# Kernel tuning notes

Hardware: AMD Instinct MI355X
Metric: run time of the kernel (lower is better)

## Reference

```python
import jax, jax.numpy as jnp
import numpy as np

B, T, D, H = 4, 2048, 1024, 16
DK = D // H  # 64
EPS = 1e-5


def _rope(q, k, offset=0):
    # q, k: (B, H, T, DK). Standard rotate-half RoPE, base 10000.
    half = DK // 2
    inv_freq = 1.0 / (10000.0 ** (jnp.arange(0, half, dtype=jnp.float32) / half))
    pos = jnp.arange(q.shape[2], dtype=jnp.float32) + offset  # (T,)
    freqs = pos[:, None] * inv_freq[None, :]          # (T, half)
    cos = jnp.concatenate([jnp.cos(freqs)] * 2, -1)   # (T, DK)
    sin = jnp.concatenate([jnp.sin(freqs)] * 2, -1)

    def rot(x):
        x1, x2 = x[..., :half], x[..., half:]
        return jnp.concatenate([-x2, x1], axis=-1)

    q = q * cos + rot(q) * sin
    k = k * cos + rot(k) * sin
    return q, k


def setup_inputs() -> dict:
    key = jax.random.key(0)
    k0, k1, k2 = jax.random.split(key, 3)
    s = 0.02
    return {
        "x": jax.random.normal(k0, (B, T, D), jnp.float32),
        "ln_w": jnp.ones((D,), jnp.float32),
        "ln_b": jnp.zeros((D,), jnp.float32),
        "w_qkv": jax.random.normal(k1, (D, 3 * D), jnp.float32) * s,
        "b_qkv": jnp.zeros((3 * D,), jnp.float32),
        "w_o": jax.random.normal(k2, (D, D), jnp.float32) * s,
        "b_o": jnp.zeros((D,), jnp.float32),
    }


def reference(x, ln_w, ln_b, w_qkv, b_qkv, w_o, b_o):
    # LayerNorm
    mu = jnp.mean(x, axis=-1, keepdims=True)
    var = jnp.mean(jnp.square(x - mu), axis=-1, keepdims=True)
    h = (x - mu) * jax.lax.rsqrt(var + EPS) * ln_w + ln_b

    # Fused QKV projection -> (B, T, 3, H, DK) -> per-head (B, H, T, DK)
    qkv = (h @ w_qkv + b_qkv).reshape(B, T, 3, H, DK)
    q = qkv[:, :, 0].transpose(0, 2, 1, 3)
    k = qkv[:, :, 1].transpose(0, 2, 1, 3)
    v = qkv[:, :, 2].transpose(0, 2, 1, 3)

    q, k = _rope(q, k, offset=0)

    # Causal SDPA
    scale = 1.0 / np.sqrt(DK)
    scores = jnp.einsum("bhqd,bhkd->bhqk", q, k) * scale
    causal = jnp.tril(jnp.ones((T, T), dtype=bool))
    scores = jnp.where(causal, scores, jnp.finfo(scores.dtype).min)
    attn = jax.nn.softmax(scores, axis=-1)
    out = jnp.einsum("bhqk,bhkd->bhqd", attn, v)

    out = out.transpose(0, 2, 1, 3).reshape(B, T, D)
    return out @ w_o + b_o
```

## Files before the change

### kernel.cpp

```cpp
#include <hip/hip_runtime.h>
#include <math.h>

#define B_ 4
#define T_ 2048
#define D_ 1024
#define H_ 16
#define DK_ 64
#define EPS_ 1e-5f
#define LOG2E 1.44269504f

typedef __attribute__((ext_vector_type(4))) float f32x4;
typedef __attribute__((ext_vector_type(8))) short sv8;
typedef __attribute__((ext_vector_type(4))) short sv4;

__device__ __forceinline__ short f2bf(float f) {
  union { float f; unsigned u; } x; x.f = f;
  unsigned r = x.u + 0x7fffu + ((x.u >> 16) & 1u);
  return (short)(r >> 16);
}

__device__ __forceinline__ void gload16(const void* g, void* l) {
  __builtin_amdgcn_global_load_lds((const __attribute__((address_space(1))) void*)g,
                                   (__attribute__((address_space(3))) void*)l, 16, 0, 0);
}

__global__ __launch_bounds__(256) void rope_tab(float2* __restrict__ cs) {
  const int i = blockIdx.x * 256 + threadIdx.x;
  const int t = i >> 5, f = i & 31;
  const float inv = powf(10000.0f, -(float)f / 32.0f);
  float sn, cn;
  sincosf((float)t * inv, &sn, &cn);
  cs[i] = make_float2(cn, sn);
}

__global__ __launch_bounds__(256) void ln_kernel(const float* __restrict__ x,
                                                 const float* __restrict__ w,
                                                 const float* __restrict__ b,
                                                 short* __restrict__ h) {
  const int row = blockIdx.x;
  const float4 v = ((const float4*)(x + (size_t)row * D_))[threadIdx.x];
  float s  = v.x + v.y + v.z + v.w;
  float ss = v.x*v.x + v.y*v.y + v.z*v.z + v.w*v.w;
  #pragma unroll
  for (int o = 32; o > 0; o >>= 1) {
    s  += __shfl_down(s,  o);
    ss += __shfl_down(ss, o);
  }
  __shared__ float red[8];
  const int wid = threadIdx.x >> 6, lane = threadIdx.x & 63;
  if (lane == 0) { red[wid] = s; red[wid + 4] = ss; }
  __syncthreads();
  s  = red[0] + red[1] + red[2] + red[3];
  ss = red[4] + red[5] + red[6] + red[7];
  const float mu  = s * (1.0f / D_);
  const float var = ss * (1.0f / D_) - mu * mu;
  const float inv = rsqrtf(var + EPS_);
  const float4 wv = ((const float4*)w)[threadIdx.x];
  const float4 bv = ((const float4*)b)[threadIdx.x];
  sv4 o;
  o[0] = f2bf((v.x - mu) * inv * wv.x + bv.x);
  o[1] = f2bf((v.y - mu) * inv * wv.y + bv.y);
  o[2] = f2bf((v.z - mu) * inv * wv.z + bv.z);
  o[3] = f2bf((v.w - mu) * inv * wv.w + bv.w);
  ((sv4*)(h + (size_t)row * D_))[threadIdx.x] = o;
}

__global__ __launch_bounds__(256) void conv_t(const float* __restrict__ W,
                                              short* __restrict__ WT,
                                              int K, int N) {
  __shared__ float tile[32][33];
  const int k0 = blockIdx.y * 32, n0 = blockIdx.x * 32;
  const int tx = threadIdx.x & 31, ty = threadIdx.x >> 5;
  #pragma unroll
  for (int i = 0; i < 4; ++i) {
    const int k = ty * 4 + i;
    tile[k][tx] = W[(size_t)(k0 + k) * N + n0 + tx];
  }
  __syncthreads();
  #pragma unroll
  for (int i = 0; i < 4; ++i) {
    const int n = ty * 4 + i;
    WT[(size_t)(n0 + n) * K + k0 + tx] = f2bf(tile[tx][n]);
  }
}

#define GBM 128
#define GBN 128
#define GBK 32

__device__ __forceinline__ void gstage(const short* __restrict__ A,
                                       const short* __restrict__ BT,
                                       short* AsB, short* BsB,
                                       int tid, size_t aoff, size_t boff) {
  #pragma unroll
  for (int rr = 0; rr < 2; ++rr) {
    const int c = tid + rr * 256;
    const int row = c >> 2, co = (c & 3) * 8;
    gload16(A + aoff + (size_t)row * D_ + co, AsB + c * 8);
    gload16(BT + boff + (size_t)row * D_ + co, BsB + c * 8);
  }
}

__global__ __launch_bounds__(256) void gemm_qkv_rope(const short* __restrict__ A,
                                                     const short* __restrict__ BT,
                                                     const float* __restrict__ bias,
                                                     const float2* __restrict__ cs,
                                                     short* __restrict__ qb,
                                                     short* __restrict__ kb,
                                                     short* __restrict__ vt) {
  __shared__ __align__(16) short As[2][GBM][GBK];
  __shared__ __align__(16) short Bs[2][GBN][GBK];
  const int tid = threadIdx.x;
  const int l = tid & 63, g = l >> 4, lq = l & 15;
  const int wm = (tid >> 6) >> 1, wn = (tid >> 6) & 1;
  const int m0 = blockIdx.y * GBM, n0 = blockIdx.x * GBN;

  f32x4 acc[4][4] = {};

  gstage(A, BT, &As[0][0][0], &Bs[0][0][0], tid, (size_t)m0 * D_, (size_t)n0 * D_);
  int cur = 0;
  for (int k0 = 0; k0 < D_; k0 += GBK) {
    __syncthreads();
    if (k0 + GBK < D_)
      gstage(A, BT, &As[cur ^ 1][0][0], &Bs[cur ^ 1][0][0], tid,
             (size_t)m0 * D_ + k0 + GBK, (size_t)n0 * D_ + k0 + GBK);
    sv8 af[4], bf[4];
    #pragma unroll
    for (int mi = 0; mi < 4; ++mi) af[mi] = *(const sv8*)&As[cur][64 * wm + 16 * mi + lq][8 * g];
    #pragma unroll
    for (int ni = 0; ni < 4; ++ni) bf[ni] = *(const sv8*)&Bs[cur][64 * wn + 16 * ni + lq][8 * g];
    #pragma unroll
    for (int mi = 0; mi < 4; ++mi)
      #pragma unroll
      for (int ni = 0; ni < 4; ++ni)
        acc[mi][ni] = __builtin_amdgcn_mfma_f32_16x16x32_bf16(af[mi], bf[ni], acc[mi][ni], 0, 0, 0);
    cur ^= 1;
  }

  const int sec = n0 >> 10;
  if (sec < 2) {
    short* dst = (sec == 0) ? qb : kb;
    const float qs = (sec == 0) ? 0.125f * LOG2E : 1.0f;
    #pragma unroll
    for (int nA = 0; nA < 2; ++nA) {
      const int colA = n0 + 64 * wn + 16 * nA + lq;
      const float bA = bias[colA], bB = bias[colA + 32];
      const int clA = colA & 1023;
      const int f = 16 * nA + lq;
      #pragma unroll
      for (int mi = 0; mi < 4; ++mi) {
        const int rbase = m0 + 64 * wm + 16 * mi + 4 * g;
        #pragma unroll
        for (int r = 0; r < 4; ++r) {
          const int row = rbase + r, t = row & (T_ - 1);
          const float2 c_s = cs[t * 32 + f];
          const float x1 = acc[mi][nA][r] + bA;
          const float x2 = acc[mi][nA + 2][r] + bB;
          dst[(size_t)row * D_ + clA]      = f2bf((x1 * c_s.x - x2 * c_s.y) * qs);
          dst[(size_t)row * D_ + clA + 32] = f2bf((x2 * c_s.x + x1 * c_s.y) * qs);
        }
      }
    }
  } else {
    #pragma unroll
    for (int ni = 0; ni < 4; ++ni) {
      const int col = n0 + 64 * wn + 16 * ni + lq;
      const float bb = bias[col];
      const int cl = col & 1023;
      const int hh = cl >> 6, d = cl & 63;
      #pragma unroll
      for (int mi = 0; mi < 4; ++mi) {
        const int rbase = m0 + 64 * wm + 16 * mi + 4 * g;
        #pragma unroll
        for (int r = 0; r < 4; ++r) {
          const int row = rbase + r;
          const int bI = row >> 11, t = row & (T_ - 1);
          vt[((size_t)(bI * H_ + hh) * DK_ + d) * T_ + t] = f2bf(acc[mi][ni][r] + bb);
        }
      }
    }
  }
}

__global__ __launch_bounds__(256) void gemm_bf16(const short* __restrict__ A,
                                                 const short* __restrict__ BT,
                                                 const float* __restrict__ bias,
                                                 float* __restrict__ C,
                                                 int M, int N) {
  __shared__ __align__(16) short As[2][GBM][GBK];
  __shared__ __align__(16) short Bs[2][GBN][GBK];
  const int tid = threadIdx.x;
  const int l = tid & 63, g = l >> 4, lq = l & 15;
  const int wm = (tid >> 6) >> 1, wn = (tid >> 6) & 1;
  const int m0 = blockIdx.y * GBM, n0 = blockIdx.x * GBN;

  f32x4 acc[4][4] = {};

  gstage(A, BT, &As[0][0][0], &Bs[0][0][0], tid, (size_t)m0 * D_, (size_t)n0 * D_);
  int cur = 0;
  for (int k0 = 0; k0 < D_; k0 += GBK) {
    __syncthreads();
    if (k0 + GBK < D_)
      gstage(A, BT, &As[cur ^ 1][0][0], &Bs[cur ^ 1][0][0], tid,
             (size_t)m0 * D_ + k0 + GBK, (size_t)n0 * D_ + k0 + GBK);
    sv8 af[4], bf[4];
    #pragma unroll
    for (int mi = 0; mi < 4; ++mi) af[mi] = *(const sv8*)&As[cur][64 * wm + 16 * mi + lq][8 * g];
    #pragma unroll
    for (int ni = 0; ni < 4; ++ni) bf[ni] = *(const sv8*)&Bs[cur][64 * wn + 16 * ni + lq][8 * g];
    #pragma unroll
    for (int mi = 0; mi < 4; ++mi)
      #pragma unroll
      for (int ni = 0; ni < 4; ++ni)
        acc[mi][ni] = __builtin_amdgcn_mfma_f32_16x16x32_bf16(af[mi], bf[ni], acc[mi][ni], 0, 0, 0);
    cur ^= 1;
  }

  #pragma unroll
  for (int ni = 0; ni < 4; ++ni) {
    const int col = n0 + 64 * wn + 16 * ni + lq;
    const float bb = bias[col];
    #pragma unroll
    for (int mi = 0; mi < 4; ++mi) {
      const int rbase = m0 + 64 * wm + 16 * mi + 4 * g;
      #pragma unroll
      for (int r = 0; r < 4; ++r)
        C[(size_t)(rbase + r) * N + col] = acc[mi][ni][r] + bb;
    }
  }
}

__global__ __launch_bounds__(256) void flash_mfma(const short* __restrict__ qb,
                                                  const short* __restrict__ kb,
                                                  const short* __restrict__ vt,
                                                  short* __restrict__ out) {
  __shared__ __align__(16) short Ks[64][72];
  __shared__ __align__(16) short Vt[64][72];
  __shared__ __align__(16) short Ps[4][16][72];

  const int tid = threadIdx.x;
  const int w = tid >> 6, l = tid & 63, g = l >> 4, lq = l & 15;
  const int wg = blockIdx.x;
  const int pair = wg & 63, bx = wg >> 6;
  const int hh = pair & 15, b = pair >> 4;
  const int q0 = bx * 64;
  const int qrow = q0 + 16 * w + lq;

  const short* qp = qb + (size_t)(b * T_ + qrow) * D_ + hh * DK_;
  sv8 qf[2];
  qf[0] = *(const sv8*)(qp + 8 * g);
  qf[1] = *(const sv8*)(qp + 32 + 8 * g);

  f32x4 o[4] = {{0,0,0,0},{0,0,0,0},{0,0,0,0},{0,0,0,0}};
  float m_run = -INFINITY, l_run = 0.0f;

  const short* kbB = kb + (size_t)(b * T_) * D_ + hh * DK_;
  const short* vtB = vt + (size_t)(b * H_ + hh) * DK_ * T_;
  const int niter = bx + 1;

  const int skey = tid >> 3, sj = tid & 7;

  int4 kr0, kr1, vr0, vr1;
  {
    kr0 = *(const int4*)(kbB + (size_t)(skey)      * D_ + sj * 8);
    kr1 = *(const int4*)(kbB + (size_t)(skey + 32) * D_ + sj * 8);
    vr0 = *(const int4*)(vtB + (size_t)(skey)      * T_ + sj * 8);
    vr1 = *(const int4*)(vtB + (size_t)(skey + 32) * T_ + sj * 8);
  }

  for (int it = 0; it < niter; ++it) {
    const int kv0 = it * 64;
    __syncthreads();
    *(int4*)&Ks[skey][sj * 8]      = kr0;
    *(int4*)&Ks[skey + 32][sj * 8] = kr1;
    *(int4*)&Vt[skey][sj * 8]      = vr0;
    *(int4*)&Vt[skey + 32][sj * 8] = vr1;
    __syncthreads();

    if (it + 1 < niter) {
      const int nk = kv0 + 64;
      kr0 = *(const int4*)(kbB + (size_t)(nk + skey)      * D_ + sj * 8);
      kr1 = *(const int4*)(kbB + (size_t)(nk + skey + 32) * D_ + sj * 8);
      vr0 = *(const int4*)(vtB + (size_t)(skey)      * T_ + nk + sj * 8);
      vr1 = *(const int4*)(vtB + (size_t)(skey + 32) * T_ + nk + sj * 8);
    }

    float sv[4][4];
    #pragma unroll
    for (int kt = 0; kt < 4; ++kt) {
      f32x4 acc = {0, 0, 0, 0};
      #pragma unroll
      for (int s = 0; s < 2; ++s) {
        const sv8 kf = *(const sv8*)&Ks[kt * 16 + lq][32 * s + 8 * g];
        acc = __builtin_amdgcn_mfma_f32_16x16x32_bf16(kf, qf[s], acc, 0, 0, 0);
      }
      sv[kt][0] = acc[0]; sv[kt][1] = acc[1]; sv[kt][2] = acc[2]; sv[kt][3] = acc[3];
    }

    if (it == niter - 1) {
      #pragma unroll
      for (int kt = 0; kt < 4; ++kt)
        #pragma unroll
        for (int r = 0; r < 4; ++r) {
          const int key_abs = kv0 + kt * 16 + 4 * g + r;
          if (key_abs > qrow) sv[kt][r] = -INFINITY;
        }
    }

    float tm = -INFINITY;
    #pragma unroll
    for (int kt = 0; kt < 4; ++kt)
      #pragma unroll
      for (int r = 0; r < 4; ++r) tm = fmaxf(tm, sv[kt][r]);
    tm = fmaxf(tm, __shfl_xor(tm, 16));
    tm = fmaxf(tm, __shfl_xor(tm, 32));
    if (__any(tm > m_run + 8.0f)) {
      const float mn = fmaxf(m_run, tm);
      const float alpha = __builtin_amdgcn_exp2f(m_run - mn);
      l_run *= alpha;
      #pragma unroll
      for (int r = 0; r < 4; ++r) {
        const float ar = __shfl(alpha, 4 * g + r);
        o[0][r] *= ar; o[1][r] *= ar; o[2][r] *= ar; o[3][r] *= ar;
      }
      m_run = mn;
    }
    float psum = 0.0f;
    #pragma unroll
    for (int kt = 0; kt < 4; ++kt)
      #pragma unroll
      for (int r = 0; r < 4; ++r) {
        const float p = __builtin_amdgcn_exp2f(sv[kt][r] - m_run);
        sv[kt][r] = p;
        psum += p;
      }
    psum += __shfl_xor(psum, 16);
    psum += __shfl_xor(psum, 32);
    l_run += psum;

    #pragma unroll
    for (int kt = 0; kt < 4; ++kt) {
      unsigned pa_, pb_;
      asm("v_cvt_pk_bf16_f32 %0, %1, %2" : "=v"(pa_) : "v"(sv[kt][0]), "v"(sv[kt][1]));
      asm("v_cvt_pk_bf16_f32 %0, %1, %2" : "=v"(pb_) : "v"(sv[kt][2]), "v"(sv[kt][3]));
      int2 pk; pk.x = (int)pa_; pk.y = (int)pb_;
      *(int2*)&Ps[w][lq][kt * 16 + 4 * g] = pk;
    }

    #pragma unroll
    for (int s = 0; s < 2; ++s) {
      const sv8 pa = *(const sv8*)&Ps[w][lq][32 * s + 8 * g];
      #pragma unroll
      for (int dt = 0; dt < 4; ++dt) {
        const sv8 vb = *(const sv8*)&Vt[dt * 16 + lq][32 * s + 8 * g];
        o[dt] = __builtin_amdgcn_mfma_f32_16x16x32_bf16(pa, vb, o[dt], 0, 0, 0);
      }
    }
  }

  #pragma unroll
  for (int r = 0; r < 4; ++r) {
    const float li = __shfl(l_run, 4 * g + r);
    const float inv = 1.0f / li;
    const int qr = q0 + 16 * w + 4 * g + r;
    short* op = out + (size_t)(b * T_ + qr) * D_ + hh * DK_;
    #pragma unroll
    for (int dt = 0; dt < 4; ++dt)
      op[dt * 16 + lq] = f2bf(o[dt][r] * inv);
  }
}

extern "C" void kernel_launch(void* const* d_in, const int* in_sizes, int n_in,
                              void* d_out, int out_size, void* d_ws, size_t ws_size,
                              hipStream_t stream) {
  const float* x     = (const float*)d_in[0];
  const float* ln_w  = (const float*)d_in[1];
  const float* ln_b  = (const float*)d_in[2];
  const float* w_qkv = (const float*)d_in[3];
  const float* b_qkv = (const float*)d_in[4];
  const float* w_o   = (const float*)d_in[5];
  const float* b_o   = (const float*)d_in[6];
  float* outp = (float*)d_out;

  const int rows = B_ * T_;
  const size_t nHD = (size_t)rows * D_;

  short* h      = (short*)d_ws;
  short* qb     = h + nHD;
  short* kb     = qb + nHD;
  short* vt     = kb + nHD;
  short* att    = vt + nHD;
  short* wqkvT  = att + nHD;
  short* woT    = wqkvT + (size_t)D_ * 3 * D_;
  float2* csT   = (float2*)(woT + (size_t)D_ * D_);

  rope_tab<<<T_ * 32 / 256, 256, 0, stream>>>(csT);
  conv_t<<<dim3(3 * D_ / 32, D_ / 32), 256, 0, stream>>>(w_qkv, wqkvT, D_, 3 * D_);
  conv_t<<<dim3(D_ / 32, D_ / 32), 256, 0, stream>>>(w_o, woT, D_, D_);

  ln_kernel<<<rows, 256, 0, stream>>>(x, ln_w, ln_b, h);

  {
    dim3 grid(3 * D_ / GBN, rows / GBM);
    gemm_qkv_rope<<<grid, 256, 0, stream>>>(h, wqkvT, b_qkv, csT, qb, kb, vt);
  }

  {
    flash_mfma<<<(T_ / 64) * H_ * B_, 256, 0, stream>>>(qb, kb, vt, att);
  }

  {
    dim3 grid(D_ / GBN, rows / GBM);
    gemm_bf16<<<grid, 256, 0, stream>>>(att, woT, b_o, outp, rows, D_);
  }
}
```

Baseline: 305.3 us.

## Process 128 query rows per flash block and schedule longest blocks first

Each attention workgroup now handles 128 query rows (two 16-row sub-tiles per wave) instead of 64, so every K/V tile staged in LDS is reused by twice as many queries and the grid halves. Blocks are also launched in reverse query order so the longest causal blocks start first, which helps load balance. Sub-tiles that lie entirely above the diagonal are skipped, and masking is applied only on diagonal-crossing tiles. The trade-off is more registers per thread and fewer blocks to spread across the CUs.

```diff
diff --git a/kernel.cpp b/kernel.cpp
--- a/kernel.cpp
+++ b/kernel.cpp
@@ -241,22 +241,27 @@
   const int tid = threadIdx.x;
   const int w = tid >> 6, l = tid & 63, g = l >> 4, lq = l & 15;
   const int wg = blockIdx.x;
-  const int pair = wg & 63, bx = wg >> 6;
+  const int pair = wg & 63;
+  const int bx = (T_ / 128 - 1) - (wg >> 6);
   const int hh = pair & 15, b = pair >> 4;
-  const int q0 = bx * 64;
-  const int qrow = q0 + 16 * w + lq;
-
-  const short* qp = qb + (size_t)(b * T_ + qrow) * D_ + hh * DK_;
-  sv8 qf[2];
-  qf[0] = *(const sv8*)(qp + 8 * g);
-  qf[1] = *(const sv8*)(qp + 32 + 8 * g);
-
-  f32x4 o[4] = {{0,0,0,0},{0,0,0,0},{0,0,0,0},{0,0,0,0}};
-  float m_run = -INFINITY, l_run = 0.0f;
+  const int q0 = bx * 128;
+  const int rw = q0 + 32 * w;
+
+  sv8 qf[2][2];
+  #pragma unroll
+  for (int h = 0; h < 2; ++h) {
+    const short* qp = qb + (size_t)(b * T_ + rw + 16 * h + lq) * D_ + hh * DK_;
+    qf[h][0] = *(const sv8*)(qp + 8 * g);
+    qf[h][1] = *(const sv8*)(qp + 32 + 8 * g);
+  }
+
+  f32x4 o[2][4] = {};
+  float m_run[2] = {-INFINITY, -INFINITY};
+  float l_run[2] = {0.0f, 0.0f};
 
   const short* kbB = kb + (size_t)(b * T_) * D_ + hh * DK_;
   const short* vtB = vt + (size_t)(b * H_ + hh) * DK_ * T_;
-  const int niter = bx + 1;
+  const int niter = 2 * bx + 2;
 
   const int skey = tid >> 3, sj = tid & 7;
 
@@ -285,88 +290,98 @@
       vr1 = *(const int4*)(vtB + (size_t)(skey + 32) * T_ + nk + sj * 8);
     }
 
-    float sv[4][4];
-    #pragma unroll
-    for (int kt = 0; kt < 4; ++kt) {
-      f32x4 acc = {0, 0, 0, 0};
+    #pragma unroll
+    for (int h = 0; h < 2; ++h) {
+      const int rmin = rw + 16 * h;
+      if (kv0 > rmin + 15) continue;
+      const int qrow = rmin + lq;
+
+      float sv[4][4];
+      #pragma unroll
+      for (int kt = 0; kt < 4; ++kt) {
+        f32x4 acc = {0, 0, 0, 0};
+        #pragma unroll
+        for (int s = 0; s < 2; ++s) {
+          const sv8 kf = *(const sv8*)&Ks[kt * 16 + lq][32 * s + 8 * g];
+          acc = __builtin_amdgcn_mfma_f32_16x16x32_bf16(kf, qf[h][s], acc, 0, 0, 0);
+        }
+        sv[kt][0] = acc[0]; sv[kt][1] = acc[1]; sv[kt][2] = acc[2]; sv[kt][3] = acc[3];
+      }
+
+      if (kv0 + 63 > rmin) {
+        #pragma unroll
+        for (int kt = 0; kt < 4; ++kt)
+          #pragma unroll
+          for (int r = 0; r < 4; ++r) {
+            const int key_abs = kv0 + kt * 16 + 4 * g + r;
+            if (key_abs > qrow) sv[kt][r] = -INFINITY;
+          }
+      }
+
+      float tm = -INFINITY;
+      #pragma unroll
+      for (int kt = 0; kt < 4; ++kt)
+        #pragma unroll
+        for (int r = 0; r < 4; ++r) tm = fmaxf(tm, sv[kt][r]);
+      tm = fmaxf(tm, __shfl_xor(tm, 16));
+      tm = fmaxf(tm, __shfl_xor(tm, 32));
+      if (__any(tm > m_run[h] + 8.0f)) {
+        const float mn = fmaxf(m_run[h], tm);
+        const float alpha = __builtin_amdgcn_exp2f(m_run[h] - mn);
+        l_run[h] *= alpha;
+        #pragma unroll
+        for (int r = 0; r < 4; ++r) {
+          const float ar = __shfl(alpha, 4 * g + r);
+          o[h][0][r] *= ar; o[h][1][r] *= ar; o[h][2][r] *= ar; o[h][3][r] *= ar;
+        }
+        m_run[h] = mn;
+      }
+      float psum = 0.0f;
+      #pragma unroll
+      for (int kt = 0; kt < 4; ++kt)
+        #pragma unroll
+        for (int r = 0; r < 4; ++r) {
+          const float p = __builtin_amdgcn_exp2f(sv[kt][r] - m_run[h]);
+          sv[kt][r] = p;
+          psum += p;
+        }
+      psum += __shfl_xor(psum, 16);
+      psum += __shfl_xor(psum, 32);
+      l_run[h] += psum;
+
+      #pragma unroll
+      for (int kt = 0; kt < 4; ++kt) {
+        unsigned pa_, pb_;
+        asm("v_cvt_pk_bf16_f32 %0, %1, %2" : "=v"(pa_) : "v"(sv[kt][0]), "v"(sv[kt][1]));
+        asm("v_cvt_pk_bf16_f32 %0, %1, %2" : "=v"(pb_) : "v"(sv[kt][2]), "v"(sv[kt][3]));
+        int2 pk; pk.x = (int)pa_; pk.y = (int)pb_;
+        *(int2*)&Ps[w][lq][kt * 16 + 4 * g] = pk;
+      }
+
       #pragma unroll
       for (int s = 0; s < 2; ++s) {
-        const sv8 kf = *(const sv8*)&Ks[kt * 16 + lq][32 * s + 8 * g];
-        acc = __builtin_amdgcn_mfma_f32_16x16x32_bf16(kf, qf[s], acc, 0, 0, 0);
-      }
-      sv[kt][0] = acc[0]; sv[kt][1] = acc[1]; sv[kt][2] = acc[2]; sv[kt][3] = acc[3];
-    }
-
-    if (it == niter - 1) {
-      #pragma unroll
-      for (int kt = 0; kt < 4; ++kt)
-        #pragma unroll
-        for (int r = 0; r < 4; ++r) {
-          const int key_abs = kv0 + kt * 16 + 4 * g + r;
-          if (key_abs > qrow) sv[kt][r] = -INFINITY;
-        }
-    }
-
-    float tm = -INFINITY;
-    #pragma unroll
-    for (int kt = 0; kt < 4; ++kt)
-      #pragma unroll
-      for (int r = 0; r < 4; ++r) tm = fmaxf(tm, sv[kt][r]);
-    tm = fmaxf(tm, __shfl_xor(tm, 16));
-    tm = fmaxf(tm, __shfl_xor(tm, 32));
-    if (__any(tm > m_run + 8.0f)) {
-      const float mn = fmaxf(m_run, tm);
-      const float alpha = __builtin_amdgcn_exp2f(m_run - mn);
-      l_run *= alpha;
-      #pragma unroll
-      for (int r = 0; r < 4; ++r) {
-        const float ar = __shfl(alpha, 4 * g + r);
-        o[0][r] *= ar; o[1][r] *= ar; o[2][r] *= ar; o[3][r] *= ar;
-      }
-      m_run = mn;
-    }
-    float psum = 0.0f;
-    #pragma unroll
-    for (int kt = 0; kt < 4; ++kt)
-      #pragma unroll
-      for (int r = 0; r < 4; ++r) {
-        const float p = __builtin_amdgcn_exp2f(sv[kt][r] - m_run);
-        sv[kt][r] = p;
-        psum += p;
-      }
-    psum += __shfl_xor(psum, 16);
-    psum += __shfl_xor(psum, 32);
-    l_run += psum;
-
-    #pragma unroll
-    for (int kt = 0; kt < 4; ++kt) {
-      unsigned pa_, pb_;
-      asm("v_cvt_pk_bf16_f32 %0, %1, %2" : "=v"(pa_) : "v"(sv[kt][0]), "v"(sv[kt][1]));
-      asm("v_cvt_pk_bf16_f32 %0, %1, %2" : "=v"(pb_) : "v"(sv[kt][2]), "v"(sv[kt][3]));
-      int2 pk; pk.x = (int)pa_; pk.y = (int)pb_;
-      *(int2*)&Ps[w][lq][kt * 16 + 4 * g] = pk;
-    }
-
-    #pragma unroll
-    for (int s = 0; s < 2; ++s) {
-      const sv8 pa = *(const sv8*)&Ps[w][lq][32 * s + 8 * g];
-      #pragma unroll
-      for (int dt = 0; dt < 4; ++dt) {
-        const sv8 vb = *(const sv8*)&Vt[dt * 16 + lq][32 * s + 8 * g];
-        o[dt] = __builtin_amdgcn_mfma_f32_16x16x32_bf16(pa, vb, o[dt], 0, 0, 0);
-      }
-    }
-  }
-
-  #pragma unroll
-  for (int r = 0; r < 4; ++r) {
-    const float li = __shfl(l_run, 4 * g + r);
-    const float inv = 1.0f / li;
-    const int qr = q0 + 16 * w + 4 * g + r;
-    short* op = out + (size_t)(b * T_ + qr) * D_ + hh * DK_;
-    #pragma unroll
-    for (int dt = 0; dt < 4; ++dt)
-      op[dt * 16 + lq] = f2bf(o[dt][r] * inv);
+        const sv8 pa = *(const sv8*)&Ps[w][lq][32 * s + 8 * g];
+        #pragma unroll
+        for (int dt = 0; dt < 4; ++dt) {
+          const sv8 vb = *(const sv8*)&Vt[dt * 16 + lq][32 * s + 8 * g];
+          o[h][dt] = __builtin_amdgcn_mfma_f32_16x16x32_bf16(pa, vb, o[h][dt], 0, 0, 0);
+        }
+      }
+    }
+  }
+
+  #pragma unroll
+  for (int h = 0; h < 2; ++h) {
+    #pragma unroll
+    for (int r = 0; r < 4; ++r) {
+      const float li = __shfl(l_run[h], 4 * g + r);
+      const float inv = 1.0f / li;
+      const int qr = rw + 16 * h + 4 * g + r;
+      short* op = out + (size_t)(b * T_ + qr) * D_ + hh * DK_;
+      #pragma unroll
+      for (int dt = 0; dt < 4; ++dt)
+        op[dt * 16 + lq] = f2bf(o[h][dt][r] * inv);
+    }
   }
 }
 
@@ -406,7 +421,7 @@
   }
 
   {
-    flash_mfma<<<(T_ / 64) * H_ * B_, 256, 0, stream>>>(qb, kb, vt, att);
+    flash_mfma<<<(T_ / 128) * H_ * B_, 256, 0, stream>>>(qb, kb, vt, att);
   }
 
   {
```

Result: no change. 309.0 us (+1.2%).
